# Performance work log

Hardware: AMD Instinct MI355X
Metric: run time of the kernel (lower is better)

## Reference

```python
import jax, jax.numpy as jnp
import numpy as np

B, H, S, D = 4, 16, 2048, 128

def setup_inputs() -> dict:
    key = jax.random.key(0)
    kq, kk, kv = jax.random.split(key, 3)
    q = jax.random.normal(kq, (B, H, S, D), dtype=jnp.float32)
    k = jax.random.normal(kk, (B, H, S, D), dtype=jnp.float32)
    v = jax.random.normal(kv, (B, H, S, D), dtype=jnp.float32)
    return {"q": q, "k": k, "v": v}

def reference(q, k, v):
    # scores: [B, H, S, S] -- NOTE: original module applies no 1/sqrt(D) scale
    scores = jnp.einsum("bhqd,bhkd->bhqk", q, k)
    a = jax.nn.softmax(scores, axis=-1)  # numerically stable softmax
    return jnp.einsum("bhqk,bhkd->bhqd", a, v)
```

## Files before the change

kernel.cpp:

```cpp
#include <hip/hip_runtime.h>
#include <hip/hip_bf16.h>


#define QBLK   128
#define KVBLK  64
#define DHEAD  128
#define SEQ    2048
#define NT     (SEQ / KVBLK)
#define KPAD   136
#define PPAD   72
#define RESCALE_THR 8.0f

typedef _Float16 f16x8 __attribute__((ext_vector_type(8)));
typedef _Float16 f16x4 __attribute__((ext_vector_type(4)));
typedef float    f32x4 __attribute__((ext_vector_type(4)));

#define AS1P(x) ((const __attribute__((address_space(1))) void*)(size_t)(x))
#define AS3P(x) ((__attribute__((address_space(3))) void*)(unsigned long long)(unsigned)(size_t)(x))

__global__ __launch_bounds__(256)
void preconv_kernel(const float* __restrict__ K, const float* __restrict__ V,
                    _Float16* __restrict__ Kp, _Float16* __restrict__ Vp) {
    const int bt = blockIdx.x;
    const size_t src = (size_t)bt * (KVBLK * DHEAD);
    const float* Kt = K + src;
    const float* Vt = V + src;
    _Float16* Ko = Kp + src;
    _Float16* Vo = Vp + src;
    #pragma unroll
    for (int j = 0; j < 4; ++j) {
        const int c = threadIdx.x + 256 * j;
        {
            const int row = c >> 4;
            const int d0  = (c & 15) * 8;
            float4 f0 = *(const float4*)(Kt + row * DHEAD + d0);
            float4 f1 = *(const float4*)(Kt + row * DHEAD + d0 + 4);
            f16x8 h;
            h[0]=(_Float16)f0.x; h[1]=(_Float16)f0.y; h[2]=(_Float16)f0.z; h[3]=(_Float16)f0.w;
            h[4]=(_Float16)f1.x; h[5]=(_Float16)f1.y; h[6]=(_Float16)f1.z; h[7]=(_Float16)f1.w;
            *(f16x8*)&Ko[row * 128 + (d0 ^ ((row & 7) << 3))] = h;
        }
        {
            const int d   = c & 127;
            const int kvg = c >> 7;
            f16x8 h;
            #pragma unroll
            for (int i = 0; i < 8; ++i)
                h[i] = (_Float16)Vt[(kvg * 8 + i) * DHEAD + d];
            *(f16x8*)&Vo[d * 64 + ((kvg * 8) ^ ((d & 7) << 3))] = h;
        }
    }
}

__global__ __launch_bounds__(512, 2)
void attn_fwd_kernel(const float* __restrict__ Q, const _Float16* __restrict__ Kp,
                     const _Float16* __restrict__ Vp, float* __restrict__ O) {
    __shared__ __align__(16) _Float16 K_lds[2][KVBLK * DHEAD];
    __shared__ __align__(16) _Float16 V_lds[2][KVBLK * DHEAD];
    __shared__ __align__(16) _Float16 P_lds[8 * 16 * 64];

    const int tid  = threadIdx.x;
    const int lane = tid & 63;
    const int wave = tid >> 6;
    const int g    = lane >> 4;
    const int lg   = lane & 15;

    const int flat    = blockIdx.x + gridDim.x * blockIdx.y;
    const int newflat = (flat & 7) * 128 + (flat >> 3);
    const int qtile   = newflat & 15;
    const int bh      = newflat >> 4;

    const float* Qg = Q + (size_t)bh * SEQ * DHEAD + (size_t)(qtile * QBLK) * DHEAD;
    float*       Og = O + (size_t)bh * SEQ * DHEAD + (size_t)(qtile * QBLK) * DHEAD;

    f16x8 qf[4];
    {
        const float* qrow = Qg + (size_t)(wave * 16 + lg) * DHEAD;
        #pragma unroll
        for (int dc = 0; dc < 4; ++dc) {
            const int d0 = dc * 32 + g * 8;
            float4 f0 = *(const float4*)(qrow + d0);
            float4 f1 = *(const float4*)(qrow + d0 + 4);
            qf[dc][0] = (_Float16)f0.x; qf[dc][1] = (_Float16)f0.y;
            qf[dc][2] = (_Float16)f0.z; qf[dc][3] = (_Float16)f0.w;
            qf[dc][4] = (_Float16)f1.x; qf[dc][5] = (_Float16)f1.y;
            qf[dc][6] = (_Float16)f1.z; qf[dc][7] = (_Float16)f1.w;
        }
    }

    f32x4 acc[8];
    #pragma unroll
    for (int dt = 0; dt < 8; ++dt) { acc[dt][0]=0.f; acc[dt][1]=0.f; acc[dt][2]=0.f; acc[dt][3]=0.f; }
    float m = -1e30f, l = 0.f;

    #define STAGE(B, T) {                                                          \
        const _Float16* Ktile = Kp + (size_t)(bh * 32 + (T)) * (KVBLK * DHEAD);    \
        const _Float16* Vtile = Vp + (size_t)(bh * 32 + (T)) * (KVBLK * DHEAD);    \
        _Pragma("unroll")                                                          \
        for (int i = 0; i < 2; ++i) {                                              \
            const int eoff = wave * 1024 + i * 512;                                \
            __builtin_amdgcn_global_load_lds(AS1P(Ktile + eoff + lane * 8),        \
                                             AS3P(&K_lds[B][eoff]), 16, 0, 0);     \
            __builtin_amdgcn_global_load_lds(AS1P(Vtile + eoff + lane * 8),        \
                                             AS3P(&V_lds[B][eoff]), 16, 0, 0);     \
        }                                                                          \
    }

    #define COMPUTE(B) {                                                           \
        f32x4 s[4];                                                                \
        __builtin_amdgcn_s_setprio(1);                                             \
        _Pragma("unroll")                                                          \
        for (int ct = 0; ct < 4; ++ct) {                                           \
            f32x4 a; a[0]=0.f; a[1]=0.f; a[2]=0.f; a[3]=0.f;                       \
            _Pragma("unroll")                                                      \
            for (int dc = 0; dc < 4; ++dc) {                                       \
                const int krow = ct * 16 + lg;                                     \
                const int ko = krow * 128 + ((dc * 32 + g * 8) ^ ((krow & 7) << 3)); \
                f16x8 kh = *(const f16x8*)&K_lds[B][ko];                           \
                a = __builtin_amdgcn_mfma_f32_16x16x32_f16(kh, qf[dc], a, 0, 0, 0);\
            }                                                                      \
            s[ct] = a;                                                             \
        }                                                                          \
        __builtin_amdgcn_s_setprio(0);                                             \
        float pmax = s[0][0];                                                      \
        _Pragma("unroll")                                                          \
        for (int ct = 0; ct < 4; ++ct)                                             \
            _Pragma("unroll")                                                      \
            for (int r = 0; r < 4; ++r)                                            \
                pmax = fmaxf(pmax, s[ct][r]);                                      \
        pmax = fmaxf(pmax, __shfl_xor(pmax, 16));                                  \
        pmax = fmaxf(pmax, __shfl_xor(pmax, 32));                                  \
        if (!__all(pmax - m <= RESCALE_THR)) {                                     \
            const float mnew = fmaxf(m, pmax);                                     \
            const float sc   = __expf(m - mnew);                                   \
            m = mnew;                                                              \
            l *= sc;                                                               \
            _Pragma("unroll")                                                      \
            for (int r = 0; r < 4; ++r) {                                          \
                const float scr = __shfl(sc, g * 20 + r);                          \
                _Pragma("unroll")                                                  \
                for (int dt = 0; dt < 8; ++dt) acc[dt][r] *= scr;                  \
            }                                                                      \
        }                                                                          \
        float rs = 0.f;                                                            \
        _Pragma("unroll")                                                          \
        for (int ct = 0; ct < 4; ++ct)                                             \
            _Pragma("unroll")                                                      \
            for (int r = 0; r < 4; ++r) {                                          \
                float p = __expf(s[ct][r] - m);                                    \
                s[ct][r] = p;                                                      \
                rs += p;                                                           \
            }                                                                      \
        rs += __shfl_xor(rs, 16);                                                  \
        rs += __shfl_xor(rs, 32);                                                  \
        l += rs;                                                                   \
        _Float16* pbase = &P_lds[wave * 16 * 64];                                  \
        _Pragma("unroll")                                                          \
        for (int ct = 0; ct < 4; ++ct) {                                           \
            f16x4 pk;                                                              \
            pk[0] = (_Float16)s[ct][0]; pk[1] = (_Float16)s[ct][1];                \
            pk[2] = (_Float16)s[ct][2]; pk[3] = (_Float16)s[ct][3];                \
            *(f16x4*)&pbase[lg * 64 + ((ct * 16 + g * 4) ^ ((lg & 7) << 3))] = pk; \
        }                                                                          \
        __builtin_amdgcn_s_setprio(1);                                             \
        _Pragma("unroll")                                                          \
        for (int kt = 0; kt < 2; ++kt) {                                           \
            const int koff = (kt * 32 + g * 8) ^ ((lg & 7) << 3);                  \
            f16x8 pf = *(const f16x8*)&pbase[lg * 64 + koff];                      \
            _Pragma("unroll")                                                      \
            for (int dt = 0; dt < 8; ++dt) {                                       \
                f16x8 vf = *(const f16x8*)&V_lds[B][(dt * 16 + lg) * 64 + koff];   \
                acc[dt] = __builtin_amdgcn_mfma_f32_16x16x32_f16(pf, vf, acc[dt], 0, 0, 0); \
            }                                                                      \
        }                                                                          \
        __builtin_amdgcn_s_setprio(0);                                             \
    }

    STAGE(0, 0);
    __syncthreads();

    #pragma unroll 1
    for (int tt = 0; tt < NT / 2; ++tt) {
        const int t0 = tt * 2;
        STAGE(1, t0 + 1);
        COMPUTE(0);
        __syncthreads();
        if (t0 + 2 < NT) STAGE(0, t0 + 2);
        COMPUTE(1);
        __syncthreads();
    }

    #undef STAGE
    #undef COMPUTE

    const float linv = 1.f / l;
    float inv[4];
    #pragma unroll
    for (int r = 0; r < 4; ++r) inv[r] = __shfl(linv, g * 20 + r);
    float* ob = Og + (size_t)(wave * 16) * DHEAD;
    #pragma unroll
    for (int dt = 0; dt < 8; ++dt)
        #pragma unroll
        for (int r = 0; r < 4; ++r)
            ob[(size_t)(g * 4 + r) * DHEAD + dt * 16 + lg] = acc[dt][r] * inv[r];
}

__global__ __launch_bounds__(256, 3)
void attn_fwd_legacy(const float* __restrict__ Q, const float* __restrict__ K,
                     const float* __restrict__ V, float* __restrict__ O) {
    __shared__ __align__(16) _Float16 K_lds[KVBLK * KPAD];
    __shared__ __align__(16) _Float16 V_lds[KVBLK * DHEAD];
    __shared__ __align__(16) _Float16 P_lds[4 * 16 * PPAD];

    const int tid  = threadIdx.x;
    const int lane = tid & 63;
    const int wave = tid >> 6;
    const int g    = lane >> 4;
    const int lg   = lane & 15;

    const int flat    = blockIdx.x + gridDim.x * blockIdx.y;
    const int newflat = (flat & 7) * 256 + (flat >> 3);
    const int qtile   = newflat & 31;
    const int bh      = newflat >> 5;

    const size_t base = (size_t)bh * SEQ * DHEAD;
    const float* Qg = Q + base + (size_t)(qtile * 64) * DHEAD;
    const float* Kg = K + base;
    const float* Vg = V + base;
    float*       Og = O + base + (size_t)(qtile * 64) * DHEAD;

    const unsigned trbase = (unsigned)(size_t)&V_lds[0] + (unsigned)(g * 2048 + lg * 8);

    f16x8 qf[4];
    {
        const float* qrow = Qg + (size_t)(wave * 16 + lg) * DHEAD;
        #pragma unroll
        for (int dc = 0; dc < 4; ++dc) {
            const int d0 = dc * 32 + g * 8;
            float4 f0 = *(const float4*)(qrow + d0);
            float4 f1 = *(const float4*)(qrow + d0 + 4);
            qf[dc][0] = (_Float16)f0.x; qf[dc][1] = (_Float16)f0.y;
            qf[dc][2] = (_Float16)f0.z; qf[dc][3] = (_Float16)f0.w;
            qf[dc][4] = (_Float16)f1.x; qf[dc][5] = (_Float16)f1.y;
            qf[dc][6] = (_Float16)f1.z; qf[dc][7] = (_Float16)f1.w;
        }
    }

    f32x4 acc[8];
    #pragma unroll
    for (int dt = 0; dt < 8; ++dt) { acc[dt][0]=0.f; acc[dt][1]=0.f; acc[dt][2]=0.f; acc[dt][3]=0.f; }
    float m = -1e30f, l = 0.f;

    for (int t = 0; t < NT; ++t) {
        {
            const float* Kt = Kg + (size_t)t * KVBLK * DHEAD;
            #pragma unroll
            for (int j = 0; j < 4; ++j) {
                const int c   = tid + 256 * j;
                const int row = c >> 4;
                const int dc  = (c & 15) * 8;
                float4 f0 = *(const float4*)(Kt + row * DHEAD + dc);
                float4 f1 = *(const float4*)(Kt + row * DHEAD + dc + 4);
                f16x8 vh;
                vh[0]=(_Float16)f0.x; vh[1]=(_Float16)f0.y; vh[2]=(_Float16)f0.z; vh[3]=(_Float16)f0.w;
                vh[4]=(_Float16)f1.x; vh[5]=(_Float16)f1.y; vh[6]=(_Float16)f1.z; vh[7]=(_Float16)f1.w;
                *(f16x8*)&K_lds[row * KPAD + dc] = vh;
            }
            const float* Vt = Vg + (size_t)t * KVBLK * DHEAD;
            #pragma unroll
            for (int j = 0; j < 4; ++j) {
                const int c   = tid + 256 * j;
                const int d8  = (c & 1) | (((c >> 3) & 7) << 1);
                const int row = ((c >> 1) & 3) | ((c >> 6) << 2);
                const int d0  = d8 * 8;
                float4 f0 = *(const float4*)(Vt + row * DHEAD + d0);
                float4 f1 = *(const float4*)(Vt + row * DHEAD + d0 + 4);
                f16x8 vv;
                vv[0]=(_Float16)f0.x; vv[1]=(_Float16)f0.y; vv[2]=(_Float16)f0.z; vv[3]=(_Float16)f0.w;
                vv[4]=(_Float16)f1.x; vv[5]=(_Float16)f1.y; vv[6]=(_Float16)f1.z; vv[7]=(_Float16)f1.w;
                const int st = (row >> 2) * 8 + (d0 >> 4);
                *(f16x8*)&V_lds[st * 64 + (row & 3) * 16 + (d0 & 15)] = vv;
            }
        }
        __syncthreads();

        f32x4 s[4];
        __builtin_amdgcn_s_setprio(1);
        #pragma unroll
        for (int ct = 0; ct < 4; ++ct) {
            f32x4 a; a[0]=0.f; a[1]=0.f; a[2]=0.f; a[3]=0.f;
            #pragma unroll
            for (int dc = 0; dc < 4; ++dc) {
                const int off = (ct * 16 + lg) * KPAD + dc * 32 + g * 8;
                f16x8 kh = *(const f16x8*)&K_lds[off];
                a = __builtin_amdgcn_mfma_f32_16x16x32_f16(kh, qf[dc], a, 0, 0, 0);
            }
            s[ct] = a;
        }
        __builtin_amdgcn_s_setprio(0);

        float pmax = s[0][0];
        #pragma unroll
        for (int ct = 0; ct < 4; ++ct)
            #pragma unroll
            for (int r = 0; r < 4; ++r)
                pmax = fmaxf(pmax, s[ct][r]);
        pmax = fmaxf(pmax, __shfl_xor(pmax, 16));
        pmax = fmaxf(pmax, __shfl_xor(pmax, 32));
        const float mnew = fmaxf(m, pmax);
        const float sc   = __expf(m - mnew);
        m = mnew;
        float rs = 0.f;
        #pragma unroll
        for (int ct = 0; ct < 4; ++ct)
            #pragma unroll
            for (int r = 0; r < 4; ++r) {
                float p = __expf(s[ct][r] - mnew);
                s[ct][r] = p;
                rs += p;
            }
        rs += __shfl_xor(rs, 16);
        rs += __shfl_xor(rs, 32);
        l = l * sc + rs;

        #pragma unroll
        for (int r = 0; r < 4; ++r) {
            const float scr = __shfl(sc, g * 20 + r);
            #pragma unroll
            for (int dt = 0; dt < 8; ++dt) acc[dt][r] *= scr;
        }

        _Float16* pbase = &P_lds[wave * 16 * PPAD];
        #pragma unroll
        for (int ct = 0; ct < 4; ++ct) {
            f16x4 pk;
            pk[0] = (_Float16)s[ct][0]; pk[1] = (_Float16)s[ct][1];
            pk[2] = (_Float16)s[ct][2]; pk[3] = (_Float16)s[ct][3];
            *(f16x4*)&pbase[lg * PPAD + ct * 16 + g * 4] = pk;
        }

        #pragma unroll
        for (int kt = 0; kt < 2; ++kt) {
            f16x8 pf = *(const f16x8*)&pbase[lg * PPAD + kt * 32 + g * 8];
            #pragma unroll
            for (int dp = 0; dp < 4; ++dp) {
                f16x4 a0, a1, b0, b1;
                asm volatile(
                    "ds_read_b64_tr_b16 %0, %4 offset:%5\n\t"
                    "ds_read_b64_tr_b16 %1, %4 offset:%6\n\t"
                    "ds_read_b64_tr_b16 %2, %4 offset:%7\n\t"
                    "ds_read_b64_tr_b16 %3, %4 offset:%8\n\t"
                    "s_waitcnt lgkmcnt(0)"
                    : "=&v"(a0), "=&v"(a1), "=&v"(b0), "=&v"(b1)
                    : "v"(trbase),
                      "i"(kt * 8192 + (dp * 2 + 0) * 128),
                      "i"(kt * 8192 + 1024 + (dp * 2 + 0) * 128),
                      "i"(kt * 8192 + (dp * 2 + 1) * 128),
                      "i"(kt * 8192 + 1024 + (dp * 2 + 1) * 128)
                    : "memory");
                __builtin_amdgcn_sched_barrier(0);
                f16x8 vf0 = __builtin_shufflevector(a0, a1, 0, 1, 2, 3, 4, 5, 6, 7);
                f16x8 vf1 = __builtin_shufflevector(b0, b1, 0, 1, 2, 3, 4, 5, 6, 7);
                __builtin_amdgcn_s_setprio(1);
                acc[dp * 2 + 0] = __builtin_amdgcn_mfma_f32_16x16x32_f16(pf, vf0, acc[dp * 2 + 0], 0, 0, 0);
                acc[dp * 2 + 1] = __builtin_amdgcn_mfma_f32_16x16x32_f16(pf, vf1, acc[dp * 2 + 1], 0, 0, 0);
                __builtin_amdgcn_s_setprio(0);
            }
        }
        __syncthreads();
    }

    const float linv = 1.f / l;
    float inv[4];
    #pragma unroll
    for (int r = 0; r < 4; ++r) inv[r] = __shfl(linv, g * 20 + r);
    float* ob = Og + (size_t)(wave * 16) * DHEAD;
    #pragma unroll
    for (int dt = 0; dt < 8; ++dt)
        #pragma unroll
        for (int r = 0; r < 4; ++r)
            ob[(size_t)(g * 4 + r) * DHEAD + dt * 16 + lg] = acc[dt][r] * inv[r];
}

extern "C" void kernel_launch(void* const* d_in, const int* in_sizes, int n_in,
                              void* d_out, int out_size, void* d_ws, size_t ws_size,
                              hipStream_t stream) {
    const float* q = (const float*)d_in[0];
    const float* k = (const float*)d_in[1];
    const float* v = (const float*)d_in[2];
    float* out = (float*)d_out;
    const int BH = in_sizes[0] / (SEQ * DHEAD);

    const size_t elems = (size_t)BH * SEQ * DHEAD;
    const size_t need  = elems * 2 * sizeof(_Float16);
    if (ws_size >= need) {
        _Float16* Kp = (_Float16*)d_ws;
        _Float16* Vp = Kp + elems;
        preconv_kernel<<<dim3(BH * (SEQ / KVBLK)), dim3(256), 0, stream>>>(k, v, Kp, Vp);
        attn_fwd_kernel<<<dim3(SEQ / QBLK, BH), dim3(512), 0, stream>>>(q, Kp, Vp, out);
    } else {
        attn_fwd_legacy<<<dim3(SEQ / 64, BH), dim3(256), 0, stream>>>(q, k, v, out);
    }
}
```

Before: 222.4 us.

## Switch attention to 32x32x16 MFMA with register-resident P and 4-wave blocks

```diff
diff --git a/kernel.cpp b/kernel.cpp
--- a/kernel.cpp
+++ b/kernel.cpp
@@ -2,7 +2,6 @@
 #include <hip/hip_bf16.h>
 
 
-#define QBLK   128
 #define KVBLK  64
 #define DHEAD  128
 #define SEQ    2048
@@ -13,7 +12,8 @@
 
 typedef _Float16 f16x8 __attribute__((ext_vector_type(8)));
 typedef _Float16 f16x4 __attribute__((ext_vector_type(4)));
-typedef float    f32x4 __attribute__((ext_vector_type(4)));
+typedef float    f32x4  __attribute__((ext_vector_type(4)));
+typedef float    f32x16 __attribute__((ext_vector_type(16)));
 
 #define AS1P(x) ((const __attribute__((address_space(1))) void*)(size_t)(x))
 #define AS3P(x) ((__attribute__((address_space(3))) void*)(unsigned long long)(unsigned)(size_t)(x))
@@ -41,44 +41,46 @@
             *(f16x8*)&Ko[row * 128 + (d0 ^ ((row & 7) << 3))] = h;
         }
         {
-            const int d   = c & 127;
-            const int kvg = c >> 7;
+            const int d  = c & 127;
+            const int G  = c >> 7;
+            const int kt = G >> 1, hh = G & 1;
             f16x8 h;
             #pragma unroll
-            for (int i = 0; i < 8; ++i)
-                h[i] = (_Float16)Vt[(kvg * 8 + i) * DHEAD + d];
-            *(f16x8*)&Vo[d * 64 + ((kvg * 8) ^ ((d & 7) << 3))] = h;
+            for (int i = 0; i < 8; ++i) {
+                const int kv = kt * 16 + 4 * hh + (i & 3) + 8 * (i >> 2);
+                h[i] = (_Float16)Vt[kv * DHEAD + d];
+            }
+            *(f16x8*)&Vo[d * 64 + (G ^ (d & 7)) * 8] = h;
         }
     }
 }
 
-__global__ __launch_bounds__(512, 2)
-void attn_fwd_kernel(const float* __restrict__ Q, const _Float16* __restrict__ Kp,
-                     const _Float16* __restrict__ Vp, float* __restrict__ O) {
+__global__ __launch_bounds__(256, 2)
+void attn_fwd_kernel32(const float* __restrict__ Q, const _Float16* __restrict__ Kp,
+                       const _Float16* __restrict__ Vp, float* __restrict__ O) {
     __shared__ __align__(16) _Float16 K_lds[2][KVBLK * DHEAD];
     __shared__ __align__(16) _Float16 V_lds[2][KVBLK * DHEAD];
-    __shared__ __align__(16) _Float16 P_lds[8 * 16 * 64];
 
     const int tid  = threadIdx.x;
     const int lane = tid & 63;
     const int wave = tid >> 6;
-    const int g    = lane >> 4;
-    const int lg   = lane & 15;
+    const int l31  = lane & 31;
+    const int l5   = lane >> 5;
 
     const int flat    = blockIdx.x + gridDim.x * blockIdx.y;
     const int newflat = (flat & 7) * 128 + (flat >> 3);
     const int qtile   = newflat & 15;
     const int bh      = newflat >> 4;
 
-    const float* Qg = Q + (size_t)bh * SEQ * DHEAD + (size_t)(qtile * QBLK) * DHEAD;
-    float*       Og = O + (size_t)bh * SEQ * DHEAD + (size_t)(qtile * QBLK) * DHEAD;
-
-    f16x8 qf[4];
+    const float* Qg = Q + (size_t)bh * SEQ * DHEAD + (size_t)(qtile * 128) * DHEAD;
+    float*       Og = O + (size_t)bh * SEQ * DHEAD + (size_t)(qtile * 128) * DHEAD;
+
+    f16x8 qf[8];
     {
-        const float* qrow = Qg + (size_t)(wave * 16 + lg) * DHEAD;
-        #pragma unroll
-        for (int dc = 0; dc < 4; ++dc) {
-            const int d0 = dc * 32 + g * 8;
+        const float* qrow = Qg + (size_t)(wave * 32 + l31) * DHEAD;
+        #pragma unroll
+        for (int dc = 0; dc < 8; ++dc) {
+            const int d0 = dc * 16 + l5 * 8;
             float4 f0 = *(const float4*)(qrow + d0);
             float4 f1 = *(const float4*)(qrow + d0 + 4);
             qf[dc][0] = (_Float16)f0.x; qf[dc][1] = (_Float16)f0.y;
@@ -88,17 +90,19 @@
         }
     }
 
-    f32x4 acc[8];
-    #pragma unroll
-    for (int dt = 0; dt < 8; ++dt) { acc[dt][0]=0.f; acc[dt][1]=0.f; acc[dt][2]=0.f; acc[dt][3]=0.f; }
+    f32x16 acc[4];
+    #pragma unroll
+    for (int dt = 0; dt < 4; ++dt)
+        #pragma unroll
+        for (int r = 0; r < 16; ++r) acc[dt][r] = 0.f;
     float m = -1e30f, l = 0.f;
 
     #define STAGE(B, T) {                                                          \
         const _Float16* Ktile = Kp + (size_t)(bh * 32 + (T)) * (KVBLK * DHEAD);    \
         const _Float16* Vtile = Vp + (size_t)(bh * 32 + (T)) * (KVBLK * DHEAD);    \
         _Pragma("unroll")                                                          \
-        for (int i = 0; i < 2; ++i) {                                              \
-            const int eoff = wave * 1024 + i * 512;                                \
+        for (int i = 0; i < 4; ++i) {                                              \
+            const int eoff = wave * 2048 + i * 512;                                \
             __builtin_amdgcn_global_load_lds(AS1P(Ktile + eoff + lane * 8),        \
                                              AS3P(&K_lds[B][eoff]), 16, 0, 0);     \
             __builtin_amdgcn_global_load_lds(AS1P(Vtile + eoff + lane * 8),        \
@@ -107,28 +111,29 @@
     }
 
     #define COMPUTE(B) {                                                           \
-        f32x4 s[4];                                                                \
+        f32x16 s[2];                                                               \
         __builtin_amdgcn_s_setprio(1);                                             \
         _Pragma("unroll")                                                          \
-        for (int ct = 0; ct < 4; ++ct) {                                           \
-            f32x4 a; a[0]=0.f; a[1]=0.f; a[2]=0.f; a[3]=0.f;                       \
-            _Pragma("unroll")                                                      \
-            for (int dc = 0; dc < 4; ++dc) {                                       \
-                const int krow = ct * 16 + lg;                                     \
-                const int ko = krow * 128 + ((dc * 32 + g * 8) ^ ((krow & 7) << 3)); \
-                f16x8 kh = *(const f16x8*)&K_lds[B][ko];                           \
-                a = __builtin_amdgcn_mfma_f32_16x16x32_f16(kh, qf[dc], a, 0, 0, 0);\
+        for (int ct = 0; ct < 2; ++ct) {                                           \
+            f32x16 a;                                                              \
+            _Pragma("unroll")                                                      \
+            for (int r = 0; r < 16; ++r) a[r] = 0.f;                               \
+            _Pragma("unroll")                                                      \
+            for (int dc = 0; dc < 8; ++dc) {                                       \
+                const int kv = ct * 32 + l31;                                      \
+                const int koff = kv * 128 + (((dc * 2 + l5) ^ (kv & 7)) * 8);      \
+                f16x8 kh = *(const f16x8*)&K_lds[B][koff];                         \
+                a = __builtin_amdgcn_mfma_f32_32x32x16_f16(kh, qf[dc], a, 0, 0, 0);\
             }                                                                      \
             s[ct] = a;                                                             \
         }                                                                          \
         __builtin_amdgcn_s_setprio(0);                                             \
         float pmax = s[0][0];                                                      \
         _Pragma("unroll")                                                          \
-        for (int ct = 0; ct < 4; ++ct)                                             \
-            _Pragma("unroll")                                                      \
-            for (int r = 0; r < 4; ++r)                                            \
+        for (int ct = 0; ct < 2; ++ct)                                             \
+            _Pragma("unroll")                                                      \
+            for (int r = 0; r < 16; ++r)                                           \
                 pmax = fmaxf(pmax, s[ct][r]);                                      \
-        pmax = fmaxf(pmax, __shfl_xor(pmax, 16));                                  \
         pmax = fmaxf(pmax, __shfl_xor(pmax, 32));                                  \
         if (!__all(pmax - m <= RESCALE_THR)) {                                     \
             const float mnew = fmaxf(m, pmax);                                     \
@@ -136,43 +141,41 @@
             m = mnew;                                                              \
             l *= sc;                                                               \
             _Pragma("unroll")                                                      \
-            for (int r = 0; r < 4; ++r) {                                          \
-                const float scr = __shfl(sc, g * 20 + r);                          \
+            for (int r = 0; r < 16; ++r) {                                         \
+                const float scr = __shfl(sc, (r & 3) + 8 * (r >> 2) + 4 * l5);     \
                 _Pragma("unroll")                                                  \
-                for (int dt = 0; dt < 8; ++dt) acc[dt][r] *= scr;                  \
+                for (int dt = 0; dt < 4; ++dt) acc[dt][r] *= scr;                  \
             }                                                                      \
         }                                                                          \
         float rs = 0.f;                                                            \
         _Pragma("unroll")                                                          \
-        for (int ct = 0; ct < 4; ++ct)                                             \
-            _Pragma("unroll")                                                      \
-            for (int r = 0; r < 4; ++r) {                                          \
+        for (int ct = 0; ct < 2; ++ct)                                             \
+            _Pragma("unroll")                                                      \
+            for (int r = 0; r < 16; ++r) {                                         \
                 float p = __expf(s[ct][r] - m);                                    \
                 s[ct][r] = p;                                                      \
                 rs += p;                                                           \
             }                                                                      \
-        rs += __shfl_xor(rs, 16);                                                  \
         rs += __shfl_xor(rs, 32);                                                  \
         l += rs;                                                                   \
-        _Float16* pbase = &P_lds[wave * 16 * 64];                                  \
-        _Pragma("unroll")                                                          \
-        for (int ct = 0; ct < 4; ++ct) {                                           \
-            f16x4 pk;                                                              \
-            pk[0] = (_Float16)s[ct][0]; pk[1] = (_Float16)s[ct][1];                \
-            pk[2] = (_Float16)s[ct][2]; pk[3] = (_Float16)s[ct][3];                \
-            *(f16x4*)&pbase[lg * 64 + ((ct * 16 + g * 4) ^ ((lg & 7) << 3))] = pk; \
-        }                                                                          \
+          \
+        f16x8 pa[4];                                                               \
+        _Pragma("unroll")                                                          \
+        for (int kt = 0; kt < 4; ++kt)                                             \
+            _Pragma("unroll")                                                      \
+            for (int i = 0; i < 8; ++i)                                            \
+                pa[kt][i] = (_Float16)s[kt >> 1][4 * (2 * (kt & 1) + (i >> 2)) + (i & 3)]; \
+                                                                           \
         __builtin_amdgcn_s_setprio(1);                                             \
         _Pragma("unroll")                                                          \
-        for (int kt = 0; kt < 2; ++kt) {                                           \
-            const int koff = (kt * 32 + g * 8) ^ ((lg & 7) << 3);                  \
-            f16x8 pf = *(const f16x8*)&pbase[lg * 64 + koff];                      \
-            _Pragma("unroll")                                                      \
-            for (int dt = 0; dt < 8; ++dt) {                                       \
-                f16x8 vf = *(const f16x8*)&V_lds[B][(dt * 16 + lg) * 64 + koff];   \
-                acc[dt] = __builtin_amdgcn_mfma_f32_16x16x32_f16(pf, vf, acc[dt], 0, 0, 0); \
+        for (int kt = 0; kt < 4; ++kt)                                             \
+            _Pragma("unroll")                                                      \
+            for (int dt = 0; dt < 4; ++dt) {                                       \
+                const int d = dt * 32 + l31;                                       \
+                const int voff = d * 64 + (((kt * 2 + l5) ^ (d & 7)) * 8);         \
+                f16x8 vf = *(const f16x8*)&V_lds[B][voff];                         \
+                acc[dt] = __builtin_amdgcn_mfma_f32_32x32x16_f16(pa[kt], vf, acc[dt], 0, 0, 0); \
             }                                                                      \
-        }                                                                          \
         __builtin_amdgcn_s_setprio(0);                                             \
     }
 
@@ -194,15 +197,16 @@
     #undef COMPUTE
 
     const float linv = 1.f / l;
-    float inv[4];
-    #pragma unroll
-    for (int r = 0; r < 4; ++r) inv[r] = __shfl(linv, g * 20 + r);
-    float* ob = Og + (size_t)(wave * 16) * DHEAD;
-    #pragma unroll
-    for (int dt = 0; dt < 8; ++dt)
-        #pragma unroll
-        for (int r = 0; r < 4; ++r)
-            ob[(size_t)(g * 4 + r) * DHEAD + dt * 16 + lg] = acc[dt][r] * inv[r];
+    float inv[16];
+    #pragma unroll
+    for (int r = 0; r < 16; ++r) inv[r] = __shfl(linv, (r & 3) + 8 * (r >> 2) + 4 * l5);
+    #pragma unroll
+    for (int dt = 0; dt < 4; ++dt)
+        #pragma unroll
+        for (int r = 0; r < 16; ++r) {
+            const int qrow = wave * 32 + (r & 3) + 8 * (r >> 2) + 4 * l5;
+            Og[(size_t)qrow * DHEAD + dt * 32 + l31] = acc[dt][r] * inv[r];
+        }
 }
 
 __global__ __launch_bounds__(256, 3)
@@ -397,7 +401,7 @@
         _Float16* Kp = (_Float16*)d_ws;
         _Float16* Vp = Kp + elems;
         preconv_kernel<<<dim3(BH * (SEQ / KVBLK)), dim3(256), 0, stream>>>(k, v, Kp, Vp);
-        attn_fwd_kernel<<<dim3(SEQ / QBLK, BH), dim3(512), 0, stream>>>(q, Kp, Vp, out);
+        attn_fwd_kernel32<<<dim3(SEQ / 128, BH), dim3(256), 0, stream>>>(q, Kp, Vp, out);
     } else {
         attn_fwd_legacy<<<dim3(SEQ / 64, BH), dim3(256), 0, stream>>>(q, k, v, out);
     }
```

Measured after the change: 213.5 us. -4.0%, faster.
